# Kernel tuning notes

Hardware: AMD Instinct MI355X
Metric: run time of the kernel (lower is better)

Reference implementation:

```python
import jax, jax.numpy as jnp
import numpy as np

K = 20  # max_similar_relations


def setup_inputs() -> dict:
    key = jax.random.key(0)
    k1, k2 = jax.random.split(key)
    B, R, D = 256, 2048, 64
    x = jax.random.normal(k1, (B, R, D), dtype=jnp.float32)
    query_rels = jax.random.randint(k2, (B,), 0, R, dtype=jnp.int32)
    return {
        "x": x,
        "query_rels": query_rels,
        # raw params as in __init__: threshold_init=0.2 -> raw=0.2*2-1=-0.6; strength_init=0.05 -> raw=0.05*5-1=-0.75
        "threshold_raw": jnp.float32(-0.6),
        "strength_raw": jnp.float32(-0.75),
        "weight_scale": jnp.float32(1.0),
        "temperature": jnp.float32(1.0),
    }


def reference(x, query_rels, threshold_raw, strength_raw, weight_scale, temperature):
    B, R, D = x.shape
    bidx = jnp.arange(B)
    threshold = jax.nn.sigmoid(threshold_raw)
    strength = jax.nn.sigmoid(strength_raw) * 0.2
    temp = jnp.clip(temperature, 0.1, 10.0)

    # F.normalize(x, p=2, dim=2)
    norms = x / jnp.maximum(jnp.linalg.norm(x, axis=2, keepdims=True), 1e-12)

    q = norms[bidx, query_rels]                      # [B, D] normalized query reprs
    sims = jnp.einsum("bd,brd->br", q, norms)        # [B, R] cosine similarities
    sims = sims.at[bidx, query_rels].set(-1.0)       # exclude self
    sim_w = jax.nn.sigmoid((sims - threshold) * 10.0)

    topv, topi = jax.lax.top_k(sims, K)              # [B, K]
    valid = (topv > threshold) & (topi != query_rels[:, None])

    # softmax over valid top-k entries only (per batch row)
    logits = jnp.where(valid, topv / temp, -1e9)
    w = jax.nn.softmax(logits, axis=1)
    w = jnp.where(valid, w, 0.0)

    sw = jnp.take_along_axis(sim_w, topi, axis=1)    # smooth sigmoid weights of selected
    combined = w * sw
    adjusted = combined * (1.0 + weight_scale * topv)
    adjusted = adjusted / (jnp.sum(adjusted, axis=1, keepdims=True) + 1e-8)

    # gather top-k normalized reprs and weighted-sum them
    top_reprs = jnp.take_along_axis(norms, jnp.broadcast_to(topi[:, :, None], (B, K, D)), axis=1)
    weighted = jnp.einsum("bk,bkd->bd", adjusted, top_reprs)  # [B, D]

    q_orig = x[bidx, query_rels]                     # original (unnormalized) query repr
    has_valid = jnp.any(valid, axis=1, keepdims=True)
    mixed = (1.0 - strength) * q_orig + strength * weighted
    new_q = jnp.where(has_valid, mixed, q_orig)

    return x.at[bidx, query_rels].set(new_q)
```

## Files before the change

### kernel.cpp

```cpp
#include <hip/hip_runtime.h>
#include <math.h>

#define KTOP 20
#define R_MAX 2048
#define SPLIT 8
#define ST 66

static_assert(sizeof(float) * (4 * 32 * ST + 64) < 36 * 1024, "LDS budget");

__global__ __launch_bounds__(256, 3) void stream_sims(
    const float* __restrict__ x,
    const int* __restrict__ qrels,
    float* __restrict__ out,
    float* __restrict__ sims,
    float* __restrict__ dns,
    int R)
{
    __shared__ float s_q[64];
    __shared__ float s_tile[4][32 * ST];

    const int blk = blockIdx.x;
    const int b = blk >> 3;
    const int s = blk & (SPLIT - 1);
    const int t = threadIdx.x;
    const int qr = qrels[b];
    const long xbase = (long)b * R * 64;
    const long sbase = (long)b * R;

    if (t < 64) {
        float v = x[xbase + (long)qr * 64 + t];
        float ss = v * v;
#pragma unroll
        for (int m = 1; m < 64; m <<= 1) ss += __shfl_xor(ss, m, 64);
        s_q[t] = v / fmaxf(sqrtf(ss), 1e-12f);
    }
    __syncthreads();

    const int wid = t >> 6, lane = t & 63;
    const int g4 = lane >> 4, l16 = lane & 15;
    const int h = lane >> 5, l32 = lane & 31;

    float4 q[8];
#pragma unroll
    for (int k = 0; k < 8; ++k) q[k] = *(const float4*)(s_q + h * 32 + k * 4);

    const int row0 = s * (R / SPLIT) + wid * 64;
    const int rA0 = row0, rB0 = row0 + 32;

    float* lds = &s_tile[wid][0];

    float4 vA[8], vB[8];
#pragma unroll
    for (int j = 0; j < 8; ++j)
        vA[j] = *(const float4*)(x + xbase + (long)(rA0 + g4 + 4 * j) * 64 + l16 * 4);
#pragma unroll
    for (int j = 0; j < 8; ++j)
        vB[j] = *(const float4*)(x + xbase + (long)(rB0 + g4 + 4 * j) * 64 + l16 * 4);

#pragma unroll
    for (int j = 0; j < 8; ++j) {
        const int r = g4 + 4 * j;
        *(float4*)(out + xbase + (long)(rA0 + r) * 64 + l16 * 4) = vA[j];
        float* p = lds + r * ST + l16 * 4;
        *(float2*)(p)     = make_float2(vA[j].x, vA[j].y);
        *(float2*)(p + 2) = make_float2(vA[j].z, vA[j].w);
    }
    {
        float dot = 0.0f, ssv = 0.0f;
        const float* rp = lds + l32 * ST + h * 32;
#pragma unroll
        for (int k = 0; k < 16; ++k) {
            float2 rv = *(const float2*)(rp + 2 * k);
            const float* qf = (const float*)&q[k >> 1];
            float qa = qf[(2 * k) & 3], qb = qf[(2 * k + 1) & 3];
            dot += rv.x * qa + rv.y * qb;
            ssv += rv.x * rv.x + rv.y * rv.y;
        }
        dot += __shfl_xor(dot, 32, 64);
        ssv += __shfl_xor(ssv, 32, 64);
        if (h == 0) {
            const int row = rA0 + l32;
            float dn = fmaxf(sqrtf(ssv), 1e-12f);
            sims[sbase + row] = (row == qr) ? -1.0f : dot / dn;
            dns[sbase + row] = dn;
        }
    }

#pragma unroll
    for (int j = 0; j < 8; ++j) {
        const int r = g4 + 4 * j;
        *(float4*)(out + xbase + (long)(rB0 + r) * 64 + l16 * 4) = vB[j];
        float* p = lds + r * ST + l16 * 4;
        *(float2*)(p)     = make_float2(vB[j].x, vB[j].y);
        *(float2*)(p + 2) = make_float2(vB[j].z, vB[j].w);
    }
    {
        float dot = 0.0f, ssv = 0.0f;
        const float* rp = lds + l32 * ST + h * 32;
#pragma unroll
        for (int k = 0; k < 16; ++k) {
            float2 rv = *(const float2*)(rp + 2 * k);
            const float* qf = (const float*)&q[k >> 1];
            float qa = qf[(2 * k) & 3], qb = qf[(2 * k + 1) & 3];
            dot += rv.x * qa + rv.y * qb;
            ssv += rv.x * rv.x + rv.y * rv.y;
        }
        dot += __shfl_xor(dot, 32, 64);
        ssv += __shfl_xor(ssv, 32, 64);
        if (h == 0) {
            const int row = rB0 + l32;
            float dn = fmaxf(sqrtf(ssv), 1e-12f);
            sims[sbase + row] = (row == qr) ? -1.0f : dot / dn;
            dns[sbase + row] = dn;
        }
    }
}

__global__ __launch_bounds__(256) void select_mix(
    const float* __restrict__ x,
    const int* __restrict__ qrels,
    const float* __restrict__ thr_raw,
    const float* __restrict__ str_raw,
    const float* __restrict__ wscale_p,
    const float* __restrict__ temp_p,
    const float* __restrict__ sims,
    const float* __restrict__ dns,
    float* __restrict__ out,
    int R)
{
    __shared__ float s_sims[R_MAX];
    __shared__ int   s_cand[R_MAX];
    __shared__ int   s_ncand;
    __shared__ float s_topv[KTOP];
    __shared__ int   s_topi[KTOP];
    __shared__ float s_dnsel[KTOP];
    __shared__ float s_adj[KTOP];
    __shared__ float s_strength;

    const int b = blockIdx.x;
    const int t = threadIdx.x;
    const int qr = qrels[b];
    const float threshold = 1.0f / (1.0f + expf(-thr_raw[0]));
    const long sbase = (long)b * R;
    const long xbase = (long)b * R * 64;

    if (t == 0) s_ncand = 0;
    __syncthreads();

    for (int i = t; i < R; i += 256) {
        float sv = sims[sbase + i];
        s_sims[i] = sv;
        if (sv > threshold) {
            int p = atomicAdd(&s_ncand, 1);
            s_cand[p] = i;
        }
    }
    __syncthreads();

    const int ncand = s_ncand;
    const int ksel = ncand < KTOP ? ncand : KTOP;

    if (t < 64) {
        float myv = 0.0f; int myi = 0;
        if (ncand > KTOP) {
            float lv[32]; int li[32];
#pragma unroll
            for (int j = 0; j < 32; ++j) {
                int i = t + 64 * j;
                if (i < ncand) { li[j] = s_cand[i]; lv[j] = s_sims[li[j]]; }
                else           { li[j] = 0x7fffffff; lv[j] = -INFINITY; }
            }
            for (int k = 0; k < KTOP; ++k) {
                float bv = -INFINITY; int bi = 0x7fffffff;
#pragma unroll
                for (int j = 0; j < 32; ++j)
                    if (lv[j] > bv || (lv[j] == bv && li[j] < bi)) { bv = lv[j]; bi = li[j]; }
#pragma unroll
                for (int m = 1; m < 64; m <<= 1) {
                    float v2 = __shfl_xor(bv, m, 64);
                    int   i2 = __shfl_xor(bi, m, 64);
                    if (v2 > bv || (v2 == bv && i2 < bi)) { bv = v2; bi = i2; }
                }
#pragma unroll
                for (int j = 0; j < 32; ++j) if (li[j] == bi) lv[j] = -INFINITY;
                if (t == k) { myv = bv; myi = bi; }
            }
        } else if (t < ksel) {
            myi = s_cand[t];
            myv = s_sims[myi];
        }
        if (t < ksel) {
            s_topv[t] = myv;
            s_topi[t] = myi;
            s_dnsel[t] = dns[sbase + myi];
        }
    }
    __syncthreads();

    if (t == 0) {
        float strength = (1.0f / (1.0f + expf(-str_raw[0]))) * 0.2f;
        float temp = fminf(fmaxf(temp_p[0], 0.1f), 10.0f);
        float wsc  = wscale_p[0];
        if (ksel > 0) {
            float m = -INFINITY;
            for (int k = 0; k < ksel; ++k) m = fmaxf(m, s_topv[k] / temp);
            float w[KTOP]; float wsum = 0.0f;
            for (int k = 0; k < ksel; ++k) { w[k] = expf(s_topv[k] / temp - m); wsum += w[k]; }
            float adj[KTOP]; float asum = 0.0f;
            for (int k = 0; k < ksel; ++k) {
                float tv = s_topv[k];
                float sw = 1.0f / (1.0f + expf(-(tv - threshold) * 10.0f));
                float a  = (w[k] / wsum) * sw * (1.0f + wsc * tv);
                adj[k] = a; asum += a;
            }
            for (int k = 0; k < ksel; ++k)
                s_adj[k] = (adj[k] / (asum + 1e-8f)) / s_dnsel[k];
        }
        s_strength = strength;
    }
    __syncthreads();

    if (t < 64 && ksel > 0) {
        const long qb = xbase + (long)qr * 64 + t;
        float qo = x[qb];
        float acc = 0.0f;
        for (int k = 0; k < ksel; ++k)
            acc += s_adj[k] * x[xbase + (long)s_topi[k] * 64 + t];
        float st = s_strength;
        out[qb] = (1.0f - st) * qo + st * acc;
    }
}

__global__ __launch_bounds__(1024) void fused_enhancer(
    const float* __restrict__ x,
    const int* __restrict__ qrels,
    const float* __restrict__ thr_raw,
    const float* __restrict__ str_raw,
    const float* __restrict__ wscale_p,
    const float* __restrict__ temp_p,
    float* __restrict__ out, int R)
{
    __shared__ float s_q[64];
    __shared__ float s_sims[R_MAX];
    __shared__ float s_dn[R_MAX];
    __shared__ int   s_cand[R_MAX];
    __shared__ int   s_ncand;
    __shared__ float s_topv[KTOP];
    __shared__ int   s_topi[KTOP];
    __shared__ float s_adj[KTOP];
    __shared__ float s_strength;

    const int b = blockIdx.x;
    const int t = threadIdx.x;
    const int qr = qrels[b];
    const float threshold = 1.0f / (1.0f + expf(-thr_raw[0]));

    if (t == 0) s_ncand = 0;

    if (t < 64) {
        float v = x[((long)b * R + qr) * 64 + t];
        float ss = v * v;
#pragma unroll
        for (int m = 1; m < 64; m <<= 1) ss += __shfl_xor(ss, m, 64);
        s_q[t] = v / fmaxf(sqrtf(ss), 1e-12f);
    }
    __syncthreads();

    const int grp = t >> 4, l16 = t & 15;
    const float4 q4 = *(const float4*)(s_q + l16 * 4);
    const long xbase = (long)b * R * 64;
    for (int row = grp; row < R; row += 64) {
        long base = xbase + (long)row * 64 + l16 * 4;
        const float4 v = *(const float4*)(x + base);
        *(float4*)(out + base) = v;
        float dot = v.x * q4.x + v.y * q4.y + v.z * q4.z + v.w * q4.w;
        float ss  = v.x * v.x + v.y * v.y + v.z * v.z + v.w * v.w;
#pragma unroll
        for (int m = 1; m < 16; m <<= 1) {
            dot += __shfl_xor(dot, m, 64);
            ss  += __shfl_xor(ss,  m, 64);
        }
        if (l16 == 0) {
            float dn  = fmaxf(sqrtf(ss), 1e-12f);
            float sim = (row == qr) ? -1.0f : dot / dn;
            s_sims[row] = sim;
            s_dn[row]   = dn;
            if (sim > threshold) {
                int p = atomicAdd(&s_ncand, 1);
                s_cand[p] = row;
            }
        }
    }
    __syncthreads();

    const int ncand = s_ncand;
    const int ksel = ncand < KTOP ? ncand : KTOP;

    if (t < 64) {
        if (ncand > KTOP) {
            float lv[32]; int li[32];
#pragma unroll
            for (int j = 0; j < 32; ++j) {
                int i = t + 64 * j;
                if (i < ncand) { li[j] = s_cand[i]; lv[j] = s_sims[li[j]]; }
                else           { li[j] = 0x7fffffff; lv[j] = -INFINITY; }
            }
            for (int k = 0; k < KTOP; ++k) {
                float bv = -INFINITY; int bi = 0x7fffffff;
#pragma unroll
                for (int j = 0; j < 32; ++j) {
                    if (lv[j] > bv || (lv[j] == bv && li[j] < bi)) { bv = lv[j]; bi = li[j]; }
                }
#pragma unroll
                for (int m = 1; m < 64; m <<= 1) {
                    float v2 = __shfl_xor(bv, m, 64);
                    int   i2 = __shfl_xor(bi, m, 64);
                    if (v2 > bv || (v2 == bv && i2 < bi)) { bv = v2; bi = i2; }
                }
#pragma unroll
                for (int j = 0; j < 32; ++j) if (li[j] == bi) lv[j] = -INFINITY;
                if (t == 0) { s_topv[k] = bv; s_topi[k] = bi; }
            }
        } else if (t == 0) {
            for (int k = 0; k < ksel; ++k) {
                int idx = s_cand[k];
                s_topi[k] = idx;
                s_topv[k] = s_sims[idx];
            }
        }
    }

    if (t == 0) {
        float strength = (1.0f / (1.0f + expf(-str_raw[0]))) * 0.2f;
        float temp = fminf(fmaxf(temp_p[0], 0.1f), 10.0f);
        float wsc  = wscale_p[0];
        if (ksel > 0) {
            float m = -INFINITY;
            for (int k = 0; k < ksel; ++k) m = fmaxf(m, s_topv[k] / temp);
            float w[KTOP]; float wsum = 0.0f;
            for (int k = 0; k < ksel; ++k) { w[k] = expf(s_topv[k] / temp - m); wsum += w[k]; }
            float adj[KTOP]; float asum = 0.0f;
            for (int k = 0; k < ksel; ++k) {
                float tv = s_topv[k];
                float sw = 1.0f / (1.0f + expf(-(tv - threshold) * 10.0f));
                float a  = (w[k] / wsum) * sw * (1.0f + wsc * tv);
                adj[k] = a; asum += a;
            }
            for (int k = 0; k < ksel; ++k)
                s_adj[k] = (adj[k] / (asum + 1e-8f)) / s_dn[s_topi[k]];
        }
        s_strength = strength;
    }
    __syncthreads();

    if (t < 64 && ksel > 0) {
        long qb = ((long)b * R + qr) * 64 + t;
        float qo = x[qb];
        float acc = 0.0f;
        for (int k = 0; k < ksel; ++k)
            acc += s_adj[k] * x[((long)b * R + s_topi[k]) * 64 + t];
        float st = s_strength;
        out[qb] = (1.0f - st) * qo + st * acc;
    }
}

extern "C" void kernel_launch(void* const* d_in, const int* in_sizes, int n_in,
                              void* d_out, int out_size, void* d_ws, size_t ws_size,
                              hipStream_t stream) {
    const float* x      = (const float*)d_in[0];
    const int*   qrels  = (const int*)d_in[1];
    const float* thr    = (const float*)d_in[2];
    const float* str    = (const float*)d_in[3];
    const float* wscale = (const float*)d_in[4];
    const float* temp   = (const float*)d_in[5];
    float* out = (float*)d_out;

    const int B = in_sizes[1];
    const int D = 64;
    const int R = in_sizes[0] / (B * D);
    (void)D;

    const size_t need = (size_t)B * R * 2 * sizeof(float);
    if (d_ws != nullptr && ws_size >= need && (R % (SPLIT * 256)) == 0 && R <= R_MAX) {
        float* sims = (float*)d_ws;
        float* dns  = sims + (size_t)B * R;
        stream_sims<<<B * SPLIT, 256, 0, stream>>>(x, qrels, out, sims, dns, R);
        select_mix<<<B, 256, 0, stream>>>(x, qrels, thr, str, wscale, temp,
                                          sims, dns, out, R);
    } else {
        fused_enhancer<<<B, 1024, 0, stream>>>(x, qrels, thr, str, wscale, temp, out, R);
    }
}
```

Before: 252.2 us.

## Split x-to-out copy into separate interleaved copy blocks with nontemporal stores

The first kernel now launches twice as many blocks, with even blocks doing a grid-strided, 8-way unrolled copy of x into out using nontemporal stores and odd blocks computing similarities without writing out. This removes the stores from the similarity path and lets copy and compute blocks run concurrently. Launch bounds change to allow four blocks per CU. The x data is still read twice, once by copy blocks and once by compute blocks, so total traffic may rise unless the second read hits in cache.

```diff
diff --git a/kernel.cpp b/kernel.cpp
--- a/kernel.cpp
+++ b/kernel.cpp
@@ -6,23 +6,59 @@
 #define SPLIT 8
 #define ST 66
 
+typedef float f4v __attribute__((ext_vector_type(4)));
+
 static_assert(sizeof(float) * (4 * 32 * ST + 64) < 36 * 1024, "LDS budget");
 
-__global__ __launch_bounds__(256, 3) void stream_sims(
+__global__ __launch_bounds__(256, 4) void stream_combined(
     const float* __restrict__ x,
     const int* __restrict__ qrels,
     float* __restrict__ out,
     float* __restrict__ sims,
     float* __restrict__ dns,
-    int R)
+    int R, long n4, int ncopy)
 {
     __shared__ float s_q[64];
     __shared__ float s_tile[4][32 * ST];
 
     const int blk = blockIdx.x;
-    const int b = blk >> 3;
-    const int s = blk & (SPLIT - 1);
+    const int role = blk & 1;
+    const int idx = blk >> 1;
     const int t = threadIdx.x;
+
+    if (role == 0) {
+        const f4v* __restrict__ src = (const f4v*)x;
+        f4v* __restrict__ dst = (f4v*)out;
+        const long stride = (long)ncopy * 256;
+        long i = (long)idx * 256 + t;
+        while (i + 7 * stride < n4) {
+            f4v v0 = src[i];
+            f4v v1 = src[i + stride];
+            f4v v2 = src[i + 2 * stride];
+            f4v v3 = src[i + 3 * stride];
+            f4v v4 = src[i + 4 * stride];
+            f4v v5 = src[i + 5 * stride];
+            f4v v6 = src[i + 6 * stride];
+            f4v v7 = src[i + 7 * stride];
+            __builtin_nontemporal_store(v0, &dst[i]);
+            __builtin_nontemporal_store(v1, &dst[i + stride]);
+            __builtin_nontemporal_store(v2, &dst[i + 2 * stride]);
+            __builtin_nontemporal_store(v3, &dst[i + 3 * stride]);
+            __builtin_nontemporal_store(v4, &dst[i + 4 * stride]);
+            __builtin_nontemporal_store(v5, &dst[i + 5 * stride]);
+            __builtin_nontemporal_store(v6, &dst[i + 6 * stride]);
+            __builtin_nontemporal_store(v7, &dst[i + 7 * stride]);
+            i += 8 * stride;
+        }
+        while (i < n4) {
+            __builtin_nontemporal_store(src[i], &dst[i]);
+            i += stride;
+        }
+        return;
+    }
+
+    const int b = idx >> 3;
+    const int s = idx & (SPLIT - 1);
     const int qr = qrels[b];
     const long xbase = (long)b * R * 64;
     const long sbase = (long)b * R;
@@ -46,7 +82,6 @@
 
     const int row0 = s * (R / SPLIT) + wid * 64;
     const int rA0 = row0, rB0 = row0 + 32;
-
     float* lds = &s_tile[wid][0];
 
     float4 vA[8], vB[8];
@@ -60,7 +95,6 @@
 #pragma unroll
     for (int j = 0; j < 8; ++j) {
         const int r = g4 + 4 * j;
-        *(float4*)(out + xbase + (long)(rA0 + r) * 64 + l16 * 4) = vA[j];
         float* p = lds + r * ST + l16 * 4;
         *(float2*)(p)     = make_float2(vA[j].x, vA[j].y);
         *(float2*)(p + 2) = make_float2(vA[j].z, vA[j].w);
@@ -89,7 +123,6 @@
 #pragma unroll
     for (int j = 0; j < 8; ++j) {
         const int r = g4 + 4 * j;
-        *(float4*)(out + xbase + (long)(rB0 + r) * 64 + l16 * 4) = vB[j];
         float* p = lds + r * ST + l16 * 4;
         *(float2*)(p)     = make_float2(vB[j].x, vB[j].y);
         *(float2*)(p + 2) = make_float2(vB[j].z, vB[j].w);
@@ -384,7 +417,10 @@
     if (d_ws != nullptr && ws_size >= need && (R % (SPLIT * 256)) == 0 && R <= R_MAX) {
         float* sims = (float*)d_ws;
         float* dns  = sims + (size_t)B * R;
-        stream_sims<<<B * SPLIT, 256, 0, stream>>>(x, qrels, out, sims, dns, R);
+        const int ncopy = B * SPLIT;
+        const long n4 = (long)B * R * 16;
+        stream_combined<<<2 * B * SPLIT, 256, 0, stream>>>(
+            x, qrels, out, sims, dns, R, n4, ncopy);
         select_mix<<<B, 256, 0, stream>>>(x, qrels, thr, str, wscale, temp,
                                           sims, dns, out, R);
     } else {
```

Result: slower. 265.5 us (+5.3%).

## Loop stream_sims over more rows per block with register double-buffering

Applied to the files above, without the earlier changes.

Reduces the row split per batch from 8 to 2 blocks, so each wave now loops over 256 rows, processing 32-row chunks while the next chunk's loads are in flight (register double buffering). The copy of x to the output now uses nontemporal stores, and occupancy hints drop from 3 to 2 blocks per CU. The aim is to amortize the per-block query normalization and keep memory loads continuously in flight. The cost is fewer blocks (512), which may hurt latency hiding and load balance.

```diff
diff --git a/kernel.cpp b/kernel.cpp
--- a/kernel.cpp
+++ b/kernel.cpp
@@ -3,12 +3,14 @@
 
 #define KTOP 20
 #define R_MAX 2048
-#define SPLIT 8
+#define SPLIT 2
 #define ST 66
 
+typedef float f4v __attribute__((ext_vector_type(4)));
+
 static_assert(sizeof(float) * (4 * 32 * ST + 64) < 36 * 1024, "LDS budget");
 
-__global__ __launch_bounds__(256, 3) void stream_sims(
+__global__ __launch_bounds__(256, 2) void stream_sims(
     const float* __restrict__ x,
     const int* __restrict__ qrels,
     float* __restrict__ out,
@@ -20,7 +22,7 @@
     __shared__ float s_tile[4][32 * ST];
 
     const int blk = blockIdx.x;
-    const int b = blk >> 3;
+    const int b = blk >> 1;
     const int s = blk & (SPLIT - 1);
     const int t = threadIdx.x;
     const int qr = qrels[b];
@@ -44,28 +46,28 @@
 #pragma unroll
     for (int k = 0; k < 8; ++k) q[k] = *(const float4*)(s_q + h * 32 + k * 4);
 
-    const int row0 = s * (R / SPLIT) + wid * 64;
-    const int rA0 = row0, rB0 = row0 + 32;
-
+    const int rowsPerBlock = R / SPLIT;
+    const int wrow0 = s * rowsPerBlock + wid * (rowsPerBlock / 4);
     float* lds = &s_tile[wid][0];
 
     float4 vA[8], vB[8];
-#pragma unroll
-    for (int j = 0; j < 8; ++j)
-        vA[j] = *(const float4*)(x + xbase + (long)(rA0 + g4 + 4 * j) * 64 + l16 * 4);
-#pragma unroll
-    for (int j = 0; j < 8; ++j)
-        vB[j] = *(const float4*)(x + xbase + (long)(rB0 + g4 + 4 * j) * 64 + l16 * 4);
-
-#pragma unroll
-    for (int j = 0; j < 8; ++j) {
-        const int r = g4 + 4 * j;
-        *(float4*)(out + xbase + (long)(rA0 + r) * 64 + l16 * 4) = vA[j];
-        float* p = lds + r * ST + l16 * 4;
-        *(float2*)(p)     = make_float2(vA[j].x, vA[j].y);
-        *(float2*)(p + 2) = make_float2(vA[j].z, vA[j].w);
-    }
-    {
+
+    auto LOAD = [&](float4 (&v)[8], int rbase) {
+#pragma unroll
+        for (int j = 0; j < 8; ++j)
+            v[j] = *(const float4*)(x + xbase + (long)(rbase + g4 + 4 * j) * 64 + l16 * 4);
+    };
+
+    auto PROCESS = [&](float4 (&v)[8], int rbase) {
+#pragma unroll
+        for (int j = 0; j < 8; ++j) {
+            const int r = g4 + 4 * j;
+            __builtin_nontemporal_store(*(const f4v*)&v[j],
+                (f4v*)(out + xbase + (long)(rbase + r) * 64 + l16 * 4));
+            float* p = lds + r * ST + l16 * 4;
+            *(float2*)(p)     = make_float2(v[j].x, v[j].y);
+            *(float2*)(p + 2) = make_float2(v[j].z, v[j].w);
+        }
         float dot = 0.0f, ssv = 0.0f;
         const float* rp = lds + l32 * ST + h * 32;
 #pragma unroll
@@ -79,40 +81,21 @@
         dot += __shfl_xor(dot, 32, 64);
         ssv += __shfl_xor(ssv, 32, 64);
         if (h == 0) {
-            const int row = rA0 + l32;
+            const int row = rbase + l32;
             float dn = fmaxf(sqrtf(ssv), 1e-12f);
             sims[sbase + row] = (row == qr) ? -1.0f : dot / dn;
             dns[sbase + row] = dn;
         }
-    }
-
-#pragma unroll
-    for (int j = 0; j < 8; ++j) {
-        const int r = g4 + 4 * j;
-        *(float4*)(out + xbase + (long)(rB0 + r) * 64 + l16 * 4) = vB[j];
-        float* p = lds + r * ST + l16 * 4;
-        *(float2*)(p)     = make_float2(vB[j].x, vB[j].y);
-        *(float2*)(p + 2) = make_float2(vB[j].z, vB[j].w);
-    }
-    {
-        float dot = 0.0f, ssv = 0.0f;
-        const float* rp = lds + l32 * ST + h * 32;
-#pragma unroll
-        for (int k = 0; k < 16; ++k) {
-            float2 rv = *(const float2*)(rp + 2 * k);
-            const float* qf = (const float*)&q[k >> 1];
-            float qa = qf[(2 * k) & 3], qb = qf[(2 * k + 1) & 3];
-            dot += rv.x * qa + rv.y * qb;
-            ssv += rv.x * rv.x + rv.y * rv.y;
-        }
-        dot += __shfl_xor(dot, 32, 64);
-        ssv += __shfl_xor(ssv, 32, 64);
-        if (h == 0) {
-            const int row = rB0 + l32;
-            float dn = fmaxf(sqrtf(ssv), 1e-12f);
-            sims[sbase + row] = (row == qr) ? -1.0f : dot / dn;
-            dns[sbase + row] = dn;
-        }
+    };
+
+    LOAD(vA, wrow0);
+    const int npairs = (rowsPerBlock / 4) / 64;
+    for (int p = 0; p < npairs; ++p) {
+        const int r0 = wrow0 + (2 * p) * 32;
+        LOAD(vB, r0 + 32);
+        PROCESS(vA, r0);
+        if (p + 1 < npairs) LOAD(vA, r0 + 64);
+        PROCESS(vB, r0 + 32);
     }
 }
 
@@ -381,7 +364,8 @@
     (void)D;
 
     const size_t need = (size_t)B * R * 2 * sizeof(float);
-    if (d_ws != nullptr && ws_size >= need && (R % (SPLIT * 256)) == 0 && R <= R_MAX) {
+    if (d_ws != nullptr && ws_size >= need && R <= R_MAX &&
+        (R % (SPLIT * 4 * 64)) == 0 && ((R / SPLIT / 4) % 64) == 0) {
         float* sims = (float*)d_ws;
         float* dns  = sims + (size_t)B * R;
         stream_sims<<<B * SPLIT, 256, 0, stream>>>(x, qrels, out, sims, dns, R);
```

Measured after the change: 259.3 us. 2.8% more time.
